# Performance work log

Measured on AMD Instinct MI355X. Metric: run time of the kernel, lower is better.

Reference implementation:

```python
import jax, jax.numpy as jnp
import numpy as np

B, C, H, W = 4, 32, 128, 256
EPS = 1e-5  # BatchNorm eps


def _conv1x1_bn(x, w, b, gamma, beta, mean, var):
    # x: [B,C,H,W]; 1x1 conv == channel matmul, fused with eval-mode BatchNorm
    y = jnp.einsum('bchw,oc->bohw', x, w) + b[None, :, None, None]
    scale = gamma / jnp.sqrt(var + EPS)
    shift = beta - mean * scale
    return y * scale[None, :, None, None] + shift[None, :, None, None]


def setup_inputs() -> dict:
    key = jax.random.key(0)
    ks = jax.random.split(key, 15)
    d = {
        'x_left': jax.random.normal(ks[0], (B, C, H, W), jnp.float32),
        'x_right': jax.random.normal(ks[1], (B, C, H, W), jnp.float32),
        'cost': jax.random.normal(ks[2], (2, B, H, W, W), jnp.float32),
        'q_w': jax.random.normal(ks[3], (C, C), jnp.float32),
        'q_b': jax.random.normal(ks[4], (C,), jnp.float32),
        'q_gamma': jax.random.uniform(ks[5], (C,), jnp.float32),
        'q_beta': jax.random.normal(ks[6], (C,), jnp.float32),
        'q_mean': jax.random.normal(ks[7], (C,), jnp.float32),
        'q_var': jax.random.uniform(ks[8], (C,), jnp.float32),
        'k_w': jax.random.normal(ks[9], (C, C), jnp.float32),
        'k_b': jax.random.normal(ks[10], (C,), jnp.float32),
        'k_gamma': jax.random.uniform(ks[11], (C,), jnp.float32),
        'k_beta': jax.random.normal(ks[12], (C,), jnp.float32),
        'k_mean': jax.random.normal(ks[13], (C,), jnp.float32),
        'k_var': jax.random.uniform(ks[14], (C,), jnp.float32),
    }
    return d


def reference(x_left, x_right, cost, q_w, q_b, q_gamma, q_beta, q_mean, q_var,
              k_w, k_b, k_gamma, k_beta, k_mean, k_var):
    b, c, h, w = x_left.shape
    cr = w // 3  # clamped_range

    # band masks: right2left keeps 0 <= i-j < cr (lower band); left2right keeps 0 <= j-i < cr
    idx = jnp.arange(w)
    diff = idx[:, None] - idx[None, :]  # [W,W] = i - j
    low_band = ((diff >= 0) & (diff < cr)).astype(x_left.dtype)
    up_band = low_band.T

    # right-to-left: Q from left, K from right
    q_l = jnp.transpose(_conv1x1_bn(x_left, q_w, q_b, q_gamma, q_beta, q_mean, q_var), (0, 2, 3, 1))   # [B,H,W,C]
    k_r = jnp.transpose(_conv1x1_bn(x_right, k_w, k_b, k_gamma, k_beta, k_mean, k_var), (0, 2, 3, 1))  # [B,H,W,C]
    s_r2l = jnp.einsum('bhic,bhjc->bhij', q_l, k_r) / c  # [B,H,W,W]
    cost_r2l = s_r2l * low_band + cost[0]

    # left-to-right: Q from right, K from left
    q_r = jnp.transpose(_conv1x1_bn(x_right, q_w, q_b, q_gamma, q_beta, q_mean, q_var), (0, 2, 3, 1))
    k_l = jnp.transpose(_conv1x1_bn(x_left, k_w, k_b, k_gamma, k_beta, k_mean, k_var), (0, 2, 3, 1))
    s_l2r = jnp.einsum('bhic,bhjc->bhij', q_r, k_l) / c
    cost_l2r = s_l2r * up_band + cost[1]

    # original returns (x_left + fea_left, x_right + fea_right, (r2l, l2r)) with fea == x
    return (x_left * 2.0, x_right * 2.0, cost_r2l, cost_l2r)
```

## Files before the change

### kernel.cpp

```cpp
#include <hip/hip_runtime.h>

#define BB 4
#define CC 32
#define HH 128
#define WW 256
#define CR 85
#define EPSF 1e-5f

#define O1_OFF 4194304
#define O2_OFF 8388608
#define O3_OFF 41943040
#define COST1_OFF (BB*HH*WW*WW)

__global__ __launch_bounds__(256, 2)
void pab_fused(const float* __restrict__ x_left, const float* __restrict__ x_right,
               const float* __restrict__ cost,
               const float* __restrict__ q_w, const float* __restrict__ q_b,
               const float* __restrict__ q_gamma, const float* __restrict__ q_beta,
               const float* __restrict__ q_mean, const float* __restrict__ q_var,
               const float* __restrict__ k_w, const float* __restrict__ k_b,
               const float* __restrict__ k_gamma, const float* __restrict__ k_beta,
               const float* __restrict__ k_mean, const float* __restrict__ k_var,
               float* __restrict__ out)
{
    __shared__ float qwt[CC][CC];
    __shared__ float kwt[CC][CC];
    __shared__ float qbf[CC], kbf[CC], qsc[CC], ksc[CC];
    __shared__ float Qls[WW][CC];
    __shared__ float Qrs[WW][CC];

    const int t   = threadIdx.x;
    const int bid = blockIdx.x;
    const int b   = bid >> 7;
    const int h   = bid & 127;

    if (t < CC) {
        float qs = q_gamma[t] * rsqrtf(q_var[t] + EPSF);
        float ks = k_gamma[t] * rsqrtf(k_var[t] + EPSF);
        qsc[t] = qs; ksc[t] = ks;
        qbf[t] = q_b[t] * qs + q_beta[t] - q_mean[t] * qs;
        kbf[t] = k_b[t] * ks + k_beta[t] - k_mean[t] * ks;
    }
    __syncthreads();
    for (int r = t; r < CC * CC; r += 256) {
        int o = r >> 5, c = r & 31;
        qwt[c][o] = q_w[r] * qsc[o];
        kwt[c][o] = k_w[r] * ksc[o];
    }
    __syncthreads();

    float ql[CC], qr[CC], kl[CC], kr[CC];
    #pragma unroll
    for (int o = 0; o < CC; ++o) {
        float qb0 = qbf[o], kb0 = kbf[o];
        ql[o] = qb0; qr[o] = qb0; kl[o] = kb0; kr[o] = kb0;
    }

    const int xbase = (b * CC * HH + h) * WW + t;
    #pragma unroll 4
    for (int c = 0; c < CC; ++c) {
        int idx = xbase + c * (HH * WW);
        float xl = x_left[idx];
        float xr = x_right[idx];
        out[idx]          = 2.0f * xl;
        out[O1_OFF + idx] = 2.0f * xr;
        #pragma unroll
        for (int o = 0; o < CC; ++o) {
            float qw = qwt[c][o];
            float kw = kwt[c][o];
            ql[o] += xl * qw;
            kl[o] += xl * kw;
            qr[o] += xr * qw;
            kr[o] += xr * kw;
        }
    }
    #pragma unroll
    for (int o = 0; o < CC; o += 4) {
        *(float4*)&Qls[t][o] = make_float4(ql[o], ql[o+1], ql[o+2], ql[o+3]);
        *(float4*)&Qrs[t][o] = make_float4(qr[o], qr[o+1], qr[o+2], qr[o+3]);
    }
    __syncthreads();

    const int rowbase = bid * (WW * WW) + t;
    const float* __restrict__ c0 = cost + rowbase;
    const float* __restrict__ c1 = cost + COST1_OFF + rowbase;
    float* __restrict__ o2 = out + O2_OFF + rowbase;
    float* __restrict__ o3 = out + O3_OFF + rowbase;

    #pragma unroll 2
    for (int i = 0; i < WW; ++i) {
        float v0 = c0[i * WW];
        float v1 = c1[i * WW];
        int d = i - t;
        if (d >= 0 && d < CR) {
            float s = 0.f;
            #pragma unroll
            for (int o = 0; o < CC; o += 4) {
                float4 q = *(const float4*)&Qls[i][o];
                s += q.x * kr[o] + q.y * kr[o+1] + q.z * kr[o+2] + q.w * kr[o+3];
            }
            v0 += s * (1.0f / 32.0f);
        }
        if (d <= 0 && d > -CR) {
            float s = 0.f;
            #pragma unroll
            for (int o = 0; o < CC; o += 4) {
                float4 q = *(const float4*)&Qrs[i][o];
                s += q.x * kl[o] + q.y * kl[o+1] + q.z * kl[o+2] + q.w * kl[o+3];
            }
            v1 += s * (1.0f / 32.0f);
        }
        o2[i * WW] = v0;
        o3[i * WW] = v1;
    }
}

extern "C" void kernel_launch(void* const* d_in, const int* in_sizes, int n_in,
                              void* d_out, int out_size, void* d_ws, size_t ws_size,
                              hipStream_t stream) {
    const float* x_left  = (const float*)d_in[0];
    const float* x_right = (const float*)d_in[1];
    const float* cost    = (const float*)d_in[2];
    const float* q_w     = (const float*)d_in[3];
    const float* q_b     = (const float*)d_in[4];
    const float* q_gamma = (const float*)d_in[5];
    const float* q_beta  = (const float*)d_in[6];
    const float* q_mean  = (const float*)d_in[7];
    const float* q_var   = (const float*)d_in[8];
    const float* k_w     = (const float*)d_in[9];
    const float* k_b     = (const float*)d_in[10];
    const float* k_gamma = (const float*)d_in[11];
    const float* k_beta  = (const float*)d_in[12];
    const float* k_mean  = (const float*)d_in[13];
    const float* k_var   = (const float*)d_in[14];
    float* out = (float*)d_out;

    pab_fused<<<dim3(BB * HH), dim3(256), 0, stream>>>(
        x_left, x_right, cost,
        q_w, q_b, q_gamma, q_beta, q_mean, q_var,
        k_w, k_b, k_gamma, k_beta, k_mean, k_var,
        out);
}
```

Before: 612.6 us.

## Split into projection and MFMA bf16 banded score kernels with workspace

```diff
diff --git a/kernel.cpp b/kernel.cpp
--- a/kernel.cpp
+++ b/kernel.cpp
@@ -9,8 +9,193 @@
 
 #define O1_OFF 4194304
 #define O2_OFF 8388608
-#define O3_OFF 41943040
-#define COST1_OFF (BB*HH*WW*WW)
+#define COST1 33554432
+
+typedef __attribute__((ext_vector_type(8))) short bf16x8;
+typedef __attribute__((ext_vector_type(4))) float f32x4;
+
+#define ARR (512 * 256 * 32)
+#define WS_Q(side) ((side) * ARR)
+#define WS_K(side) (2 * ARR + (side) * ARR)
+#define WS_NEEDED (4ull * ARR * 2ull)
+
+static __device__ __forceinline__ unsigned short f2bf(float f) {
+    unsigned u = __float_as_uint(f);
+    unsigned r = (u + 0x7FFFu + ((u >> 16) & 1u)) >> 16;
+    return (unsigned short)r;
+}
+
+__global__ __launch_bounds__(256, 4)
+void proj_kernel(const float* __restrict__ x_left, const float* __restrict__ x_right,
+                 const float* __restrict__ q_w, const float* __restrict__ q_b,
+                 const float* __restrict__ q_gamma, const float* __restrict__ q_beta,
+                 const float* __restrict__ q_mean, const float* __restrict__ q_var,
+                 const float* __restrict__ k_w, const float* __restrict__ k_b,
+                 const float* __restrict__ k_gamma, const float* __restrict__ k_beta,
+                 const float* __restrict__ k_mean, const float* __restrict__ k_var,
+                 float* __restrict__ out, unsigned short* __restrict__ ws)
+{
+    __shared__ float wq[CC][CC];
+    __shared__ float wk[CC][CC];
+    __shared__ float bq[CC], bk[CC], sq[CC], sk[CC];
+
+    const int t    = threadIdx.x;
+    const int side = blockIdx.x >> 9;
+    const int bh   = blockIdx.x & 511;
+
+    if (t < CC) {
+        float qs = q_gamma[t] * rsqrtf(q_var[t] + EPSF);
+        float ks = k_gamma[t] * rsqrtf(k_var[t] + EPSF);
+        sq[t] = qs; sk[t] = ks;
+        bq[t] = q_b[t] * qs + q_beta[t] - q_mean[t] * qs;
+        bk[t] = k_b[t] * ks + k_beta[t] - k_mean[t] * ks;
+    }
+    __syncthreads();
+    for (int r = t; r < CC * CC; r += 256) {
+        int o = r >> 5, c = r & 31;
+        wq[c][o] = q_w[r] * sq[o];
+        wk[c][o] = k_w[r] * sk[o];
+    }
+    __syncthreads();
+
+    float q[CC], k[CC];
+    #pragma unroll
+    for (int o = 0; o < CC; ++o) { q[o] = bq[o]; k[o] = bk[o]; }
+
+    const float* x = side ? x_right : x_left;
+    const int b = bh >> 7, h = bh & 127;
+    const int xbase = (b * CC * HH + h) * WW + t;
+    float* outx = out + side * O1_OFF;
+
+    #pragma unroll 4
+    for (int c = 0; c < CC; ++c) {
+        int idx = xbase + c * (HH * WW);
+        float xv = x[idx];
+        outx[idx] = 2.0f * xv;
+        #pragma unroll
+        for (int o = 0; o < CC; ++o) {
+            q[o] += xv * wq[c][o];
+            k[o] += xv * wk[c][o];
+        }
+    }
+
+    unsigned short* qdst = ws + WS_Q(side) + (bh * WW + t) * CC;
+    unsigned short* kdst = ws + WS_K(side) + (bh * WW + t) * CC;
+    #pragma unroll
+    for (int g = 0; g < 4; ++g) {
+        uint4 vq, vk;
+        vq.x = f2bf(q[8*g+0]) | ((unsigned)f2bf(q[8*g+1]) << 16);
+        vq.y = f2bf(q[8*g+2]) | ((unsigned)f2bf(q[8*g+3]) << 16);
+        vq.z = f2bf(q[8*g+4]) | ((unsigned)f2bf(q[8*g+5]) << 16);
+        vq.w = f2bf(q[8*g+6]) | ((unsigned)f2bf(q[8*g+7]) << 16);
+        vk.x = f2bf(k[8*g+0]) | ((unsigned)f2bf(k[8*g+1]) << 16);
+        vk.y = f2bf(k[8*g+2]) | ((unsigned)f2bf(k[8*g+3]) << 16);
+        vk.z = f2bf(k[8*g+4]) | ((unsigned)f2bf(k[8*g+5]) << 16);
+        vk.w = f2bf(k[8*g+6]) | ((unsigned)f2bf(k[8*g+7]) << 16);
+        ((uint4*)qdst)[g] = vq;
+        ((uint4*)kdst)[g] = vk;
+    }
+}
+
+__global__ __launch_bounds__(256, 6)
+void score_kernel(const float* __restrict__ cost, const unsigned short* __restrict__ ws,
+                  float* __restrict__ out)
+{
+    __shared__ char lds[32 * 132 * 4];
+    unsigned short* Qs = (unsigned short*)lds;
+    unsigned short* Ks = (unsigned short*)(lds + 2048);
+    float* Sb = (float*)lds;
+
+    const int t    = threadIdx.x;
+    const int bx   = blockIdx.x;
+    const int tile = bx & 7;
+    const int bh   = (bx >> 3) & 511;
+    const int dir  = bx >> 12;
+    const int i0   = tile * 32;
+    const int wbase = dir ? i0 : (i0 - 96);
+
+    const unsigned short* qsrc = ws + (dir ? WS_Q(1) : WS_Q(0)) + bh * WW * CC;
+    const unsigned short* ksrc = ws + (dir ? WS_K(0) : WS_K(1)) + bh * WW * CC;
+
+    if (t < 128) {
+        ((uint4*)Qs)[t] = ((const uint4*)(qsrc + i0 * CC))[t];
+    }
+    {
+        uint4* dst = (uint4*)Ks;
+        #pragma unroll
+        for (int qq = t; qq < 512; qq += 256) {
+            int col = wbase + (qq >> 2);
+            uint4 v = make_uint4(0u, 0u, 0u, 0u);
+            if (col >= 0 && col < WW)
+                v = ((const uint4*)(ksrc + col * CC))[qq & 3];
+            dst[qq] = v;
+        }
+    }
+    __syncthreads();
+
+    const int w = t >> 6, lane = t & 63;
+    const int quad = lane >> 4, l16 = lane & 15;
+    f32x4 acc[2][2] = {};
+    bf16x8 afrag[2], bfrag[2];
+    #pragma unroll
+    for (int mt = 0; mt < 2; ++mt)
+        afrag[mt] = *(const bf16x8*)(Qs + (16 * mt + l16) * CC + quad * 8);
+    #pragma unroll
+    for (int nt = 0; nt < 2; ++nt)
+        bfrag[nt] = *(const bf16x8*)(Ks + (32 * w + 16 * nt + l16) * CC + quad * 8);
+    #pragma unroll
+    for (int mt = 0; mt < 2; ++mt)
+        #pragma unroll
+        for (int nt = 0; nt < 2; ++nt)
+            acc[mt][nt] = __builtin_amdgcn_mfma_f32_16x16x32_bf16(
+                afrag[mt], bfrag[nt], acc[mt][nt], 0, 0, 0);
+    __syncthreads();
+
+    #pragma unroll
+    for (int mt = 0; mt < 2; ++mt)
+        #pragma unroll
+        for (int nt = 0; nt < 2; ++nt) {
+            int cl = 32 * w + 16 * nt + l16;
+            #pragma unroll
+            for (int r = 0; r < 4; ++r) {
+                int row = 16 * mt + quad * 4 + r;
+                Sb[row * 132 + cl] = acc[mt][nt][r];
+            }
+        }
+    __syncthreads();
+
+    const float* csrc = cost + (size_t)dir * COST1 + (size_t)bh * (WW * WW);
+    float* odst = out + O2_OFF + (size_t)dir * COST1 + (size_t)bh * (WW * WW);
+    const int rowlane = t >> 6;
+    const int c4 = 4 * (t & 63);
+    const float inv32 = 1.0f / 32.0f;
+
+    float4 vbuf[8];
+    #pragma unroll
+    for (int p = 0; p < 8; ++p) {
+        int rl = 4 * p + rowlane;
+        vbuf[p] = *(const float4*)(csrc + (i0 + rl) * WW + c4);
+    }
+    #pragma unroll
+    for (int p = 0; p < 8; ++p) {
+        int rl = 4 * p + rowlane;
+        int i = i0 + rl;
+        float4 v = vbuf[p];
+        int lc = c4 - wbase;
+        if (lc >= 0 && lc < 128) {
+            const float4 s = *(const float4*)(Sb + rl * 132 + lc);
+            int d0 = dir ? (c4 + 0 - i) : (i - c4 - 0);
+            int d1 = dir ? (c4 + 1 - i) : (i - c4 - 1);
+            int d2 = dir ? (c4 + 2 - i) : (i - c4 - 2);
+            int d3 = dir ? (c4 + 3 - i) : (i - c4 - 3);
+            if (d0 >= 0 && d0 < CR) v.x += s.x * inv32;
+            if (d1 >= 0 && d1 < CR) v.y += s.y * inv32;
+            if (d2 >= 0 && d2 < CR) v.z += s.z * inv32;
+            if (d3 >= 0 && d3 < CR) v.w += s.w * inv32;
+        }
+        *(float4*)(odst + i * WW + c4) = v;
+    }
+}
 
 __global__ __launch_bounds__(256, 2)
 void pab_fused(const float* __restrict__ x_left, const float* __restrict__ x_right,
@@ -55,7 +240,6 @@
         float qb0 = qbf[o], kb0 = kbf[o];
         ql[o] = qb0; qr[o] = qb0; kl[o] = kb0; kr[o] = kb0;
     }
-
     const int xbase = (b * CC * HH + h) * WW + t;
     #pragma unroll 4
     for (int c = 0; c < CC; ++c) {
@@ -83,9 +267,9 @@
 
     const int rowbase = bid * (WW * WW) + t;
     const float* __restrict__ c0 = cost + rowbase;
-    const float* __restrict__ c1 = cost + COST1_OFF + rowbase;
+    const float* __restrict__ c1 = cost + COST1 + rowbase;
     float* __restrict__ o2 = out + O2_OFF + rowbase;
-    float* __restrict__ o3 = out + O3_OFF + rowbase;
+    float* __restrict__ o3 = out + O2_OFF + COST1 + rowbase;
 
     #pragma unroll 2
     for (int i = 0; i < WW; ++i) {
@@ -135,9 +319,19 @@
     const float* k_var   = (const float*)d_in[14];
     float* out = (float*)d_out;
 
-    pab_fused<<<dim3(BB * HH), dim3(256), 0, stream>>>(
-        x_left, x_right, cost,
-        q_w, q_b, q_gamma, q_beta, q_mean, q_var,
-        k_w, k_b, k_gamma, k_beta, k_mean, k_var,
-        out);
-}
+    if (ws_size >= WS_NEEDED) {
+        unsigned short* ws = (unsigned short*)d_ws;
+        proj_kernel<<<dim3(1024), dim3(256), 0, stream>>>(
+            x_left, x_right,
+            q_w, q_b, q_gamma, q_beta, q_mean, q_var,
+            k_w, k_b, k_gamma, k_beta, k_mean, k_var,
+            out, ws);
+        score_kernel<<<dim3(8192), dim3(256), 0, stream>>>(cost, ws, out);
+    } else {
+        pab_fused<<<dim3(BB * HH), dim3(256), 0, stream>>>(
+            x_left, x_right, cost,
+            q_w, q_b, q_gamma, q_beta, q_mean, q_var,
+            k_w, k_b, k_gamma, k_beta, k_mean, k_var,
+            out);
+    }
+}
```

Result: faster. 558.9 us (-8.8%).
